# Performance work log

Hardware: AMD Instinct MI355X
Metric: run time of the kernel (lower is better)

The kernel has to match this reference:

```python
import jax, jax.numpy as jnp
import numpy as np

T, H, I, E, K, L, R = 1024, 1024, 1024, 8, 2, 4, 16
N = 2 * I  # gate_up dim


def setup_inputs() -> dict:
    key = jax.random.key(0)
    ks = jax.random.split(key, 12)
    tw = jax.random.uniform(ks[1], (T, K), dtype=jnp.float32) + 0.1
    tw = tw / tw.sum(axis=-1, keepdims=True)  # routing weights sum to 1
    return {
        "hidden_states": jax.random.normal(ks[0], (T, H), dtype=jnp.float32),
        "topk_weights": tw,
        "w13": jax.random.normal(ks[2], (E, N, H), dtype=jnp.float32) * (1.0 / np.sqrt(H)),
        "w2": jax.random.normal(ks[3], (E, H, I), dtype=jnp.float32) * (1.0 / np.sqrt(I)),
        "gate_up_lora_a": jax.random.normal(ks[4], (L, E, R, H), dtype=jnp.float32) * (1.0 / np.sqrt(H)),
        "gate_up_lora_b": jax.random.normal(ks[5], (L, E, N, R), dtype=jnp.float32) * (1.0 / np.sqrt(R)),
        "down_lora_a": jax.random.normal(ks[6], (L, E, R, I), dtype=jnp.float32) * (1.0 / np.sqrt(I)),
        "down_lora_b": jax.random.normal(ks[7], (L, E, H, R), dtype=jnp.float32) * (1.0 / np.sqrt(R)),
        "scalings": jax.random.uniform(ks[8], (L,), dtype=jnp.float32) + 0.5,
        "topk_ids": jax.random.randint(ks[9], (T, K), 0, E, dtype=jnp.int32),
        "lora_indices": jax.random.randint(ks[10], (T,), 0, L, dtype=jnp.int32),
    }


def reference(hidden_states, topk_weights, w13, w2, gate_up_lora_a,
              gate_up_lora_b, down_lora_a, down_lora_b, scalings,
              topk_ids, lora_indices):
    num_tokens, hidden = hidden_states.shape
    num_experts, gate_up_dim, _ = w13.shape
    top_k = topk_ids.shape[1]
    inter = gate_up_dim // 2
    TKp = num_tokens * top_k

    e_flat = topk_ids.reshape(-1)                      # [TK] expert per dispatched pair
    l_flat = jnp.repeat(lora_indices, top_k)           # [TK] adapter per pair
    w_flat = topk_weights.reshape(-1)                  # [TK] routing weight
    x_rep = jnp.repeat(hidden_states, top_k, axis=0)   # [TK, H]

    # ---- grouped gate_up GEMM (base path): cache1[p] = x[p] @ w13[e(p)]^T ----
    cache1 = jnp.zeros((TKp, gate_up_dim), dtype=hidden_states.dtype)
    for ei in range(num_experts):  # small fixed expert count
        mask = (e_flat == ei)[:, None]
        cache1 = cache1 + jnp.where(mask, x_rep @ w13[ei].T, 0.0)

    # ---- per-expert gate_up LoRA delta, injected BEFORE activation ----
    scal = scalings[l_flat][:, None]                   # [TK, 1]
    Ag = gate_up_lora_a[l_flat, e_flat]                # [TK, R, H]
    Bg = gate_up_lora_b[l_flat, e_flat]                # [TK, N, R]
    tmp = jnp.einsum('prh,ph->pr', Ag, x_rep)
    cache1 = cache1 + jnp.einsum('pnr,pr->pn', Bg, tmp) * scal

    # ---- silu_and_mul on (base + lora) ----
    act = jax.nn.silu(cache1[:, :inter]) * cache1[:, inter:]   # [TK, I]

    # ---- grouped down GEMM (base), routed-weight applied ----
    cache3 = jnp.zeros((TKp, hidden), dtype=hidden_states.dtype)
    for ei in range(num_experts):
        mask = (e_flat == ei)[:, None]
        cache3 = cache3 + jnp.where(mask, act @ w2[ei].T, 0.0)
    cache3 = cache3 * w_flat[:, None]

    # ---- per-expert down LoRA delta (weighted by routing weight) ----
    Ad = down_lora_a[l_flat, e_flat]                   # [TK, R, I]
    Bd = down_lora_b[l_flat, e_flat]                   # [TK, H, R]
    tmpd = jnp.einsum('pri,pi->pr', Ad, act)
    cache3 = cache3 + jnp.einsum('phr,pr->ph', Bd, tmpd) * scal * w_flat[:, None]

    # ---- combine expert outputs (moe_sum over top_k slots) ----
    return cache3.reshape(num_tokens, top_k, hidden).sum(axis=1)
```

## Files before the change

kernel.cpp:

```cpp
#include <hip/hip_runtime.h>
#include <stdint.h>

#define Td 1024
#define Hd 1024
#define Id 1024
#define Ed 8
#define Kd 2
#define Ld 4
#define Rd 16
#define Nd 2048
#define TKd (Td*Kd)

typedef __bf16 bf16x8 __attribute__((ext_vector_type(8)));
typedef float f32x4 __attribute__((ext_vector_type(4)));

__device__ __forceinline__ ushort f2bf(float f) {
    uint32_t u = __builtin_bit_cast(uint32_t, f);
    return (ushort)((u + 0x7fffu + ((u >> 16) & 1u)) >> 16);
}
__device__ __forceinline__ float bf2f(ushort u) {
    uint32_t x = ((uint32_t)u) << 16;
    return __builtin_bit_cast(float, x);
}
__device__ __forceinline__ bf16x8 pack8(float4 a, float4 b) {
    bf16x8 r;
    r[0] = (__bf16)a.x; r[1] = (__bf16)a.y; r[2] = (__bf16)a.z; r[3] = (__bf16)a.w;
    r[4] = (__bf16)b.x; r[5] = (__bf16)b.y; r[6] = (__bf16)b.z; r[7] = (__bf16)b.w;
    return r;
}
__device__ __forceinline__ void cvt16(const float* __restrict__ s, ushort* __restrict__ d) {
    float4 a0 = *(const float4*)(s);
    float4 a1 = *(const float4*)(s + 4);
    float4 a2 = *(const float4*)(s + 8);
    float4 a3 = *(const float4*)(s + 12);
    uint4 o0, o1;
    o0.x = (uint)f2bf(a0.x) | ((uint)f2bf(a0.y) << 16);
    o0.y = (uint)f2bf(a0.z) | ((uint)f2bf(a0.w) << 16);
    o0.z = (uint)f2bf(a1.x) | ((uint)f2bf(a1.y) << 16);
    o0.w = (uint)f2bf(a1.z) | ((uint)f2bf(a1.w) << 16);
    o1.x = (uint)f2bf(a2.x) | ((uint)f2bf(a2.y) << 16);
    o1.y = (uint)f2bf(a2.z) | ((uint)f2bf(a2.w) << 16);
    o1.z = (uint)f2bf(a3.x) | ((uint)f2bf(a3.y) << 16);
    o1.w = (uint)f2bf(a3.z) | ((uint)f2bf(a3.w) << 16);
    *(uint4*)(d) = o0;
    *(uint4*)(d + 8) = o1;
}

#define GLOAD_LDS16(g, l) __builtin_amdgcn_global_load_lds( \
    (const __attribute__((address_space(1))) uint32_t*)(const void*)(g), \
    (__attribute__((address_space(3))) uint32_t*)(void*)(l), 16, 0, 0)

#define W2C 2048
#define TB 2048
#define XB 256
#define CB 384
#define ZB 1024
#define PREP_BLOCKS (W2C + TB + XB + CB + ZB + 1)

__global__ __launch_bounds__(256) void k_prep(
    const float* __restrict__ hid, const float* __restrict__ w2,
    const float* __restrict__ gb, const float* __restrict__ db,
    const float* __restrict__ ga, const float* __restrict__ sc,
    const int* __restrict__ tids, const int* __restrict__ lidx,
    ushort* __restrict__ xb, ushort* __restrict__ w2b,
    ushort* __restrict__ gbbe, ushort* __restrict__ dbbe, ushort* __restrict__ tmp1e,
    float* __restrict__ out, int* __restrict__ sorted, int* __restrict__ offs)
{
    __shared__ float tr[Rd];
    __shared__ int cnt[Ed];
    __shared__ int cur[Ed];
    const int b = blockIdx.x, tid = threadIdx.x;

    if (b < W2C) {
        size_t off = ((size_t)b * 256 + tid) * 16;
        cvt16(w2 + off, w2b + off);
    } else if (b < W2C + TB) {
        const int p = b - W2C;
        const int e = tids[p];
        const int l = lidx[p >> 1];
        const float s = sc[l];
        const int r = tid >> 4, q = tid & 15;
        const float* A = ga + (((size_t)l * Ed + e) * Rd + r) * 1024;
        const float* x = hid + (size_t)(p >> 1) * 1024;
        float sum = 0.f;
        #pragma unroll
        for (int i = 0; i < 16; ++i) {
            int h = q * 4 + 64 * i;
            float4 a = *(const float4*)(A + h);
            float4 v = *(const float4*)(x + h);
            sum += a.x * v.x + a.y * v.y + a.z * v.z + a.w * v.w;
        }
        sum += __shfl_xor(sum, 1); sum += __shfl_xor(sum, 2);
        sum += __shfl_xor(sum, 4); sum += __shfl_xor(sum, 8);
        if (q == 0) tr[r] = sum;
        __syncthreads();
        if (tid < 32) {
            int j0 = tid * 2;
            uint v = 0;
            if ((j0 >> 4) == l)
                v = (uint)f2bf(s * tr[j0 & 15]) | ((uint)f2bf(s * tr[(j0 + 1) & 15]) << 16);
            ((uint*)(tmp1e + (size_t)p * 64))[tid] = v;
        }
    } else if (b < W2C + TB + XB) {
        size_t off = ((size_t)(b - W2C - TB) * 256 + tid) * 16;
        cvt16(hid + off, xb + off);
    } else if (b < W2C + TB + XB + CB) {
        constexpr int GR = Ld * Ed * Nd;
        int i = (b - W2C - TB - XB) * 256 + tid;
        const float* src; ushort* dst;
        if (i < GR) {
            int l = i >> 14, e = (i >> 11) & 7, n = i & 2047;
            src = gb + (size_t)i * 16;
            dst = gbbe + ((size_t)(e * Nd + n)) * 64 + l * 16;
        } else {
            int j = i - GR;
            int l = j >> 13, e = (j >> 10) & 7, n = j & 1023;
            src = db + (size_t)j * 16;
            dst = dbbe + ((size_t)(e * Id + n)) * 64 + l * 16;
        }
        cvt16(src, dst);
    } else if (b < W2C + TB + XB + CB + ZB) {
        int i = (b - W2C - TB - XB - CB) * 256 + tid;
        ((float4*)out)[i] = make_float4(0.f, 0.f, 0.f, 0.f);
    } else {
        if (tid < Ed) cnt[tid] = 0;
        __syncthreads();
        int el[8];
        #pragma unroll
        for (int i = 0; i < 8; ++i) {
            el[i] = tids[tid + i * 256];
            atomicAdd(&cnt[el[i]], 1);
        }
        __syncthreads();
        if (tid == 0) {
            int s = 0;
            for (int e = 0; e < Ed; ++e) { offs[e] = s; cur[e] = s; s += cnt[e]; }
            offs[Ed] = s;
        }
        __syncthreads();
        #pragma unroll
        for (int i = 0; i < 8; ++i) {
            int pos = atomicAdd(&cur[el[i]], 1);
            sorted[pos] = tid + i * 256;
        }
    }
}

__global__ __launch_bounds__(256) void k_tmp_dn(
    const ushort* __restrict__ act, const float* __restrict__ da,
    const float* __restrict__ sc, const int* __restrict__ tids,
    const int* __restrict__ lidx, ushort* __restrict__ tmpde)
{
    const int p = blockIdx.x;
    const int e = tids[p];
    const int l = lidx[p >> 1];
    const float s = sc[l];
    const int tid = threadIdx.x;
    const int r = tid >> 4, q = tid & 15;
    const float* A = da + (((size_t)l * Ed + e) * Rd + r) * 1024;
    const ushort* x = act + (size_t)p * 1024;
    float sum = 0.f;
    #pragma unroll
    for (int i = 0; i < 8; ++i) {
        int h = q * 8 + 128 * i;
        float4 a0 = *(const float4*)(A + h);
        float4 a1 = *(const float4*)(A + h + 4);
        ushort4 v0 = *(const ushort4*)(x + h);
        ushort4 v1 = *(const ushort4*)(x + h + 4);
        sum += a0.x * bf2f(v0.x) + a0.y * bf2f(v0.y) + a0.z * bf2f(v0.z) + a0.w * bf2f(v0.w)
             + a1.x * bf2f(v1.x) + a1.y * bf2f(v1.y) + a1.z * bf2f(v1.z) + a1.w * bf2f(v1.w);
    }
    sum += __shfl_xor(sum, 1); sum += __shfl_xor(sum, 2);
    sum += __shfl_xor(sum, 4); sum += __shfl_xor(sum, 8);
    __shared__ float tr[Rd];
    if (q == 0) tr[r] = sum;
    __syncthreads();
    if (tid < 32) {
        int j0 = tid * 2;
        uint v = 0;
        if ((j0 >> 4) == l)
            v = (uint)f2bf(s * tr[j0 & 15]) | ((uint)f2bf(s * tr[(j0 + 1) & 15]) << 16);
        ((uint*)(tmpde + (size_t)p * 64))[tid] = v;
    }
}

__global__ __launch_bounds__(256) void k_gemm_gu(
    const ushort* __restrict__ xb, const float* __restrict__ w13,
    const ushort* __restrict__ tmp1e, const ushort* __restrict__ gbbe,
    ushort* __restrict__ act, const int* __restrict__ sorted,
    const int* __restrict__ offs)
{
    __shared__ ushort As[2][64][32];
    __shared__ ushort Bs[2][128][32];
    const int tid = threadIdx.x, lane = tid & 63, wave = tid >> 6;
    const int wr = wave >> 1, wc = wave & 1;
    const int fr = lane & 15, fk = (lane >> 4) * 8;

    int off[Ed + 1];
    #pragma unroll
    for (int e = 0; e <= Ed; ++e) off[e] = offs[e];
    int mt[Ed]; int tot = 0;
    #pragma unroll
    for (int e = 0; e < Ed; ++e) {
        mt[e] = (off[e + 1] - off[e] + 63) / 64;
        tot += mt[e] * 16;
    }

    for (int tau = blockIdx.x; tau < tot; tau += gridDim.x) {
        int t = tau, e = 0;
        while (t >= mt[e] * 16) { t -= mt[e] * 16; ++e; }
        const int m0 = off[e] + (t >> 4) * 64;
        const int mend = off[e + 1];
        const int n0 = (t & 15) * 64;

        const ushort *asrc, *aesrc;
        {
            int aIdx = m0 + (tid >> 2); if (aIdx > mend - 1) aIdx = mend - 1;
            int p = sorted[aIdx];
            asrc  = xb + (size_t)(p >> 1) * 1024 + (tid & 3) * 8;
            aesrc = tmp1e + (size_t)p * 64 + (tid & 3) * 8;
        }
        const int brow = tid >> 1, bhalf = tid & 1;
        const int bg_row = (brow < 64) ? (n0 + brow) : (1024 + n0 + brow - 64);
        const float* bsrc = w13 + ((size_t)e * Nd + bg_row) * 1024 + bhalf * 16;
        const ushort* besrc[2];
        #pragma unroll
        for (int r = 0; r < 2; ++r) {
            int c = r * 256 + tid;
            int row = c >> 2, kc = c & 3;
            int grow = (row < 64) ? (n0 + row) : (1024 + n0 + row - 64);
            besrc[r] = gbbe + ((size_t)e * Nd + grow) * 64 + kc * 8;
        }

        f32x4 ag[2][2] = {}, au[2][2] = {};
        auto step = [&](int b) {
            bf16x8 af[2], bg[2], bu[2];
            #pragma unroll
            for (int mi = 0; mi < 2; ++mi)
                af[mi] = *(const bf16x8*)(&As[b][wr * 32 + mi * 16 + fr][fk]);
            #pragma unroll
            for (int ni = 0; ni < 2; ++ni) {
                bg[ni] = *(const bf16x8*)(&Bs[b][wc * 32 + ni * 16 + fr][fk]);
                bu[ni] = *(const bf16x8*)(&Bs[b][64 + wc * 32 + ni * 16 + fr][fk]);
            }
            #pragma unroll
            for (int mi = 0; mi < 2; ++mi)
                #pragma unroll
                for (int ni = 0; ni < 2; ++ni) {
                    ag[mi][ni] = __builtin_amdgcn_mfma_f32_16x16x32_bf16(af[mi], bg[ni], ag[mi][ni], 0, 0, 0);
                    au[mi][ni] = __builtin_amdgcn_mfma_f32_16x16x32_bf16(af[mi], bu[ni], au[mi][ni], 0, 0, 0);
                }
        };

        GLOAD_LDS16(asrc, (char*)&As[0][0][0] + (wave * 64) * 16);
        {
            float4 y0 = *(const float4*)(bsrc);
            float4 y1 = *(const float4*)(bsrc + 4);
            float4 y2 = *(const float4*)(bsrc + 8);
            float4 y3 = *(const float4*)(bsrc + 12);
            *(bf16x8*)(&Bs[0][brow][bhalf * 16])     = pack8(y0, y1);
            *(bf16x8*)(&Bs[0][brow][bhalf * 16 + 8]) = pack8(y2, y3);
        }
        __syncthreads();

        int buf = 0;
        for (int k0 = 32; k0 < 1024; k0 += 32) {
            GLOAD_LDS16(asrc + k0, (char*)&As[buf ^ 1][0][0] + (wave * 64) * 16);
            float4 y0 = *(const float4*)(bsrc + k0);
            float4 y1 = *(const float4*)(bsrc + k0 + 4);
            float4 y2 = *(const float4*)(bsrc + k0 + 8);
            float4 y3 = *(const float4*)(bsrc + k0 + 12);

            step(buf);

            *(bf16x8*)(&Bs[buf ^ 1][brow][bhalf * 16])     = pack8(y0, y1);
            *(bf16x8*)(&Bs[buf ^ 1][brow][bhalf * 16 + 8]) = pack8(y2, y3);
            __syncthreads();
            buf ^= 1;
        }
        step(buf);

        #pragma unroll
        for (int es = 0; es < 2; ++es) {
            GLOAD_LDS16(aesrc + es * 32, (char*)&As[es][0][0] + (wave * 64) * 16);
            #pragma unroll
            for (int r = 0; r < 2; ++r)
                GLOAD_LDS16(besrc[r] + es * 32, (char*)&Bs[es][0][0] + (r * 256 + wave * 64) * 16);
            __syncthreads();
            step(es);
        }

        const int rb = wr * 32 + (lane >> 4) * 4;
        #pragma unroll
        for (int mi = 0; mi < 2; ++mi) {
            #pragma unroll
            for (int j = 0; j < 4; ++j) {
                int sidx = m0 + rb + mi * 16 + j;
                if (sidx < mend) {
                    int p = sorted[sidx];
                    ushort* ar = act + (size_t)p * 1024 + n0 + wc * 32;
                    #pragma unroll
                    for (int ni = 0; ni < 2; ++ni) {
                        float g = ag[mi][ni][j], u = au[mi][ni][j];
                        float v = g / (1.f + __expf(-g)) * u;
                        ar[ni * 16 + fr] = f2bf(v);
                    }
                }
            }
        }
        __syncthreads();
    }
}

__global__ __launch_bounds__(256) void k_gemm_dn(
    const ushort* __restrict__ act, const ushort* __restrict__ w2b,
    const ushort* __restrict__ tmpde, const ushort* __restrict__ dbbe,
    const float* __restrict__ tw, float* __restrict__ out,
    const int* __restrict__ sorted, const int* __restrict__ offs)
{
    __shared__ ushort As[64][32];
    __shared__ ushort Bs[64][32];
    const int tid = threadIdx.x, lane = tid & 63, wave = tid >> 6;
    const int wr = wave >> 1, wc = wave & 1;
    const int fr = lane & 15, fk = (lane >> 4) * 8;

    int off[Ed + 1];
    #pragma unroll
    for (int e = 0; e <= Ed; ++e) off[e] = offs[e];
    int mt[Ed]; int tot = 0;
    #pragma unroll
    for (int e = 0; e < Ed; ++e) {
        mt[e] = (off[e + 1] - off[e] + 63) / 64;
        tot += mt[e] * 16;
    }

    for (int tau = blockIdx.x; tau < tot; tau += gridDim.x) {
        int t = tau, e = 0;
        while (t >= mt[e] * 16) { t -= mt[e] * 16; ++e; }
        const int m0 = off[e] + (t >> 4) * 64;
        const int mend = off[e + 1];
        const int n0 = (t & 15) * 64;

        const ushort *asrc, *aesrc, *bsrc, *besrc;
        {
            int aIdx = m0 + (tid >> 2); if (aIdx > mend - 1) aIdx = mend - 1;
            int p = sorted[aIdx];
            asrc  = act + (size_t)p * 1024 + (tid & 3) * 8;
            aesrc = tmpde + (size_t)p * 64 + (tid & 3) * 8;
            int row = tid >> 2, kc = tid & 3;
            bsrc  = w2b + ((size_t)e * Hd + n0 + row) * 1024 + kc * 8;
            besrc = dbbe + ((size_t)e * Hd + n0 + row) * 64 + kc * 8;
        }

        f32x4 acc[2][2] = {};
        auto step = [&]() {
            bf16x8 af[2], bv[2];
            #pragma unroll
            for (int mi = 0; mi < 2; ++mi)
                af[mi] = *(const bf16x8*)(&As[wr * 32 + mi * 16 + fr][fk]);
            #pragma unroll
            for (int ni = 0; ni < 2; ++ni)
                bv[ni] = *(const bf16x8*)(&Bs[wc * 32 + ni * 16 + fr][fk]);
            #pragma unroll
            for (int mi = 0; mi < 2; ++mi)
                #pragma unroll
                for (int ni = 0; ni < 2; ++ni)
                    acc[mi][ni] = __builtin_amdgcn_mfma_f32_16x16x32_bf16(af[mi], bv[ni], acc[mi][ni], 0, 0, 0);
        };

        for (int k0 = 0; k0 < 1024; k0 += 32) {
            GLOAD_LDS16(asrc + k0, (char*)&As[0][0] + (wave * 64) * 16);
            GLOAD_LDS16(bsrc + k0, (char*)&Bs[0][0] + (wave * 64) * 16);
            __syncthreads();
            step();
            __syncthreads();
        }
        #pragma unroll
        for (int es = 0; es < 2; ++es) {
            GLOAD_LDS16(aesrc + es * 32, (char*)&As[0][0] + (wave * 64) * 16);
            GLOAD_LDS16(besrc + es * 32, (char*)&Bs[0][0] + (wave * 64) * 16);
            __syncthreads();
            step();
            __syncthreads();
        }

        const int rb = wr * 32 + (lane >> 4) * 4;
        #pragma unroll
        for (int mi = 0; mi < 2; ++mi) {
            #pragma unroll
            for (int j = 0; j < 4; ++j) {
                int sidx = m0 + rb + mi * 16 + j;
                if (sidx < mend) {
                    int p = sorted[sidx];
                    float w = tw[p];
                    float* orow = out + (size_t)(p >> 1) * 1024 + n0 + wc * 32;
                    #pragma unroll
                    for (int ni = 0; ni < 2; ++ni)
                        atomicAdd(&orow[ni * 16 + fr], w * acc[mi][ni][j]);
                }
            }
        }
    }
}

extern "C" void kernel_launch(void* const* d_in, const int* in_sizes, int n_in,
                              void* d_out, int out_size, void* d_ws, size_t ws_size,
                              hipStream_t stream) {
    const float* hid  = (const float*)d_in[0];
    const float* tw   = (const float*)d_in[1];
    const float* w13  = (const float*)d_in[2];
    const float* w2   = (const float*)d_in[3];
    const float* ga   = (const float*)d_in[4];
    const float* gb   = (const float*)d_in[5];
    const float* da   = (const float*)d_in[6];
    const float* db   = (const float*)d_in[7];
    const float* sc   = (const float*)d_in[8];
    const int*   tids = (const int*)d_in[9];
    const int*   lidx = (const int*)d_in[10];
    float* out = (float*)d_out;

    char* ws = (char*)d_ws;
    ushort* xb     = (ushort*)(ws);
    ushort* w2b    = (ushort*)(ws + (2ull  << 20));
    ushort* gbbe   = (ushort*)(ws + (18ull << 20));
    ushort* dbbe   = (ushort*)(ws + (20ull << 20));
    ushort* tmp1e  = (ushort*)(ws + (21ull << 20));
    ushort* tmpde  = (ushort*)(ws + (21ull << 20) + (256u << 10));
    ushort* act    = (ushort*)(ws + (22ull << 20));
    int*    sorted = (int*)(ws + (26ull << 20));
    int*    offs   = (int*)(ws + (26ull << 20) + TKd * 4);

    k_prep<<<PREP_BLOCKS, 256, 0, stream>>>(hid, w2, gb, db, ga, sc, tids, lidx,
                                            xb, w2b, gbbe, dbbe, tmp1e, out, sorted, offs);
    k_gemm_gu<<<1024, 256, 0, stream>>>(xb, w13, tmp1e, gbbe, act, sorted, offs);
    k_tmp_dn<<<TKd, 256, 0, stream>>>(act, da, sc, tids, lidx, tmpde);
    k_gemm_dn<<<1024, 256, 0, stream>>>(act, w2b, tmpde, dbbe, tw, out, sorted, offs);
}
```

Measured before the change: 92.93 us.

## Triple-buffer gate_up GEMM main loop with explicit vmcnt waits and prefetch depth two

```diff
diff --git a/kernel.cpp b/kernel.cpp
--- a/kernel.cpp
+++ b/kernel.cpp
@@ -190,8 +190,8 @@
     ushort* __restrict__ act, const int* __restrict__ sorted,
     const int* __restrict__ offs)
 {
-    __shared__ ushort As[2][64][32];
-    __shared__ ushort Bs[2][128][32];
+    __shared__ ushort As[3][64][32];
+    __shared__ ushort Bs[3][128][32];
     const int tid = threadIdx.x, lane = tid & 63, wave = tid >> 6;
     const int wr = wave >> 1, wc = wave & 1;
     const int fr = lane & 15, fk = (lane >> 4) * 8;
@@ -233,6 +233,22 @@
         }
 
         f32x4 ag[2][2] = {}, au[2][2] = {};
+        float4 Y0[4], Y1[4];
+
+        auto issueA = [&](int s, int b) {
+            GLOAD_LDS16(asrc + s * 32, (char*)&As[b][0][0] + (wave * 64) * 16);
+        };
+        auto loadB = [&](int s, float4* Y) {
+            const float* p = bsrc + s * 32;
+            Y[0] = *(const float4*)(p);
+            Y[1] = *(const float4*)(p + 4);
+            Y[2] = *(const float4*)(p + 8);
+            Y[3] = *(const float4*)(p + 12);
+        };
+        auto writeB = [&](float4* Y, int b) {
+            *(bf16x8*)(&Bs[b][brow][bhalf * 16])     = pack8(Y[0], Y[1]);
+            *(bf16x8*)(&Bs[b][brow][bhalf * 16 + 8]) = pack8(Y[2], Y[3]);
+        };
         auto step = [&](int b) {
             bf16x8 af[2], bg[2], bu[2];
             #pragma unroll
@@ -252,34 +268,38 @@
                 }
         };
 
-        GLOAD_LDS16(asrc, (char*)&As[0][0][0] + (wave * 64) * 16);
-        {
-            float4 y0 = *(const float4*)(bsrc);
-            float4 y1 = *(const float4*)(bsrc + 4);
-            float4 y2 = *(const float4*)(bsrc + 8);
-            float4 y3 = *(const float4*)(bsrc + 12);
-            *(bf16x8*)(&Bs[0][brow][bhalf * 16])     = pack8(y0, y1);
-            *(bf16x8*)(&Bs[0][brow][bhalf * 16 + 8]) = pack8(y2, y3);
-        }
-        __syncthreads();
-
-        int buf = 0;
-        for (int k0 = 32; k0 < 1024; k0 += 32) {
-            GLOAD_LDS16(asrc + k0, (char*)&As[buf ^ 1][0][0] + (wave * 64) * 16);
-            float4 y0 = *(const float4*)(bsrc + k0);
-            float4 y1 = *(const float4*)(bsrc + k0 + 4);
-            float4 y2 = *(const float4*)(bsrc + k0 + 8);
-            float4 y3 = *(const float4*)(bsrc + k0 + 12);
-
-            step(buf);
-
-            *(bf16x8*)(&Bs[buf ^ 1][brow][bhalf * 16])     = pack8(y0, y1);
-            *(bf16x8*)(&Bs[buf ^ 1][brow][bhalf * 16 + 8]) = pack8(y2, y3);
-            __syncthreads();
-            buf ^= 1;
-        }
-        step(buf);
-
+        issueA(0, 0); loadB(0, Y0);
+        issueA(1, 1); loadB(1, Y1);
+        asm volatile("s_waitcnt vmcnt(5)" ::: "memory");
+        writeB(Y0, 0);
+
+        int b0 = 0;
+        for (int s = 0; s < 32; s += 2) {
+            int b1 = b0 + 1; if (b1 == 3) b1 = 0;
+            int b2 = b1 + 1; if (b2 == 3) b2 = 0;
+            asm volatile("s_waitcnt vmcnt(5) lgkmcnt(0)" ::: "memory");
+            __builtin_amdgcn_s_barrier();
+            __builtin_amdgcn_sched_barrier(0);
+            if (s + 2 < 32) { issueA(s + 2, b2); loadB(s + 2, Y0); }
+            step(b0);
+            if (s + 2 < 32) asm volatile("s_waitcnt vmcnt(5)" ::: "memory");
+            else            asm volatile("s_waitcnt vmcnt(0)" ::: "memory");
+            writeB(Y1, b1);
+            asm volatile("s_waitcnt vmcnt(5) lgkmcnt(0)" ::: "memory");
+            __builtin_amdgcn_s_barrier();
+            __builtin_amdgcn_sched_barrier(0);
+            if (s + 3 < 32) { issueA(s + 3, b0); loadB(s + 3, Y1); }
+            step(b1);
+            if (s + 2 < 32) {
+                if (s + 3 < 32) asm volatile("s_waitcnt vmcnt(5)" ::: "memory");
+                else            asm volatile("s_waitcnt vmcnt(0)" ::: "memory");
+                writeB(Y0, b2);
+            }
+            b0 = b2;
+        }
+
+        asm volatile("s_waitcnt vmcnt(0) lgkmcnt(0)" ::: "memory");
+        __syncthreads();
         #pragma unroll
         for (int es = 0; es < 2; ++es) {
             GLOAD_LDS16(aesrc + es * 32, (char*)&As[es][0][0] + (wave * 64) * 16);
@@ -288,6 +308,7 @@
                 GLOAD_LDS16(besrc[r] + es * 32, (char*)&Bs[es][0][0] + (r * 256 + wave * 64) * 16);
             __syncthreads();
             step(es);
+            __syncthreads();
         }
 
         const int rb = wr * 32 + (lane >> 4) * 4;
```

Measured after the change: 107.4 us. 1.16x slower.
